# Performance work log

Measured on AMD Instinct MI355X. Metric: run time of the kernel, lower is better.

The kernel has to match this reference:

```python
import jax, jax.numpy as jnp
import numpy as np

S = 4        # support_num
NEI = 32     # neighbor_num for conv stages
POOL_NEI = 4 # neighbor_num inside Pool_layer
EPS = 1e-12


def sq_dist(a, b):
    # a: (b,m,3), b: (b,n,3) -> (b,m,n)
    return (jnp.sum(a * a, -1)[:, :, None] + jnp.sum(b * b, -1)[:, None, :]
            - 2.0 * jnp.einsum('bmd,bnd->bmn', a, b))


def query_ball(radius, k, points, queries):
    # PointNet++-style ball query: up to k indices within radius, padded with first hit.
    d = sq_dist(queries, points)                      # (b,m,n)
    n = points.shape[1]
    idx = jnp.broadcast_to(jnp.arange(n, dtype=jnp.int32), d.shape)
    idx = jnp.where(d > radius * radius, n, idx)
    idx = jnp.sort(idx, axis=-1)[..., :k]             # (b,m,k)
    first = idx[..., :1]
    return jnp.where(idx == n, first, idx)


def gather_nb(feat, idx):
    # feat: (b,v,c), idx: (b,v,k) -> (b,v,k,c)
    return jax.vmap(lambda f, i: f[i])(feat, idx)


def neighbor_dir_norm(verts, idx):
    nb = gather_nb(verts, idx)                        # (b,v,k,3)
    d = nb - verts[:, :, None, :]
    return d / (jnp.linalg.norm(d, axis=-1, keepdims=True) + EPS)


def conv_surface(idx, verts, dirs):
    # dirs: (3, S*out). Geometric-only first layer of 3DGCN.
    b, v, k = idx.shape
    o = dirs.shape[1] // S
    dn = neighbor_dir_norm(verts, idx)                # (b,v,k,3)
    sd = dirs / (jnp.linalg.norm(dirs, axis=0, keepdims=True) + EPS)
    theta = jnp.maximum(jnp.einsum('bvkd,dm->bvkm', dn, sd), 0.0)
    theta = theta.reshape(b, v, k, S, o)
    return theta.max(axis=2).sum(axis=2)              # (b,v,o)


def conv_layer(idx, verts, feat, w, bias, dirs):
    # w: (cin,(S+1)*o), bias: ((S+1)*o,), dirs: (3,S*o)
    b, v, k = idx.shape
    o = dirs.shape[1] // S
    dn = neighbor_dir_norm(verts, idx)
    sd = dirs / (jnp.linalg.norm(dirs, axis=0, keepdims=True) + EPS)
    theta = jnp.maximum(jnp.einsum('bvkd,dm->bvkm', dn, sd), 0.0)  # (b,v,k,S*o)
    fout = feat @ w + bias                            # (b,v,(S+1)*o)
    center, supp = fout[..., :o], fout[..., o:]
    supp_nb = gather_nb(supp, idx)                    # (b,v,k,S*o)
    act = (theta * supp_nb).reshape(b, v, k, S, o).max(axis=2).sum(axis=2)
    return center + act


def pool(verts, feat, radius):
    idx = query_ball(radius, POOL_NEI, verts, verts)
    pooled = gather_nb(feat, idx).max(axis=2)         # (b,v,c)
    m = verts.shape[1] // 2                           # pooling_rate = 2 (deterministic subsample)
    return verts[:, :m], pooled[:, :m]


def setup_inputs() -> dict:
    key = jax.random.key(0)
    ks = jax.random.split(key, 32)
    B, V = 4, 4096
    inp = {}
    inp['vertices'] = jax.random.uniform(ks[0], (B, V, 3), dtype=jnp.float32)
    inp['surf_dirs'] = jax.random.normal(ks[1], (3, S * 32), dtype=jnp.float32) * 0.1
    specs = [(1, 32, 32), (3, 64, 32), (4, 96, 32), (6, 128, 32), (7, 160, 32),
             (8, 192, 32), (9, 224, 32), (10, 256, 32), (11, 288, 1024)]
    i = 2
    for n, cin, cout in specs:
        inp[f'w{n}'] = jax.random.normal(ks[i], (cin, (S + 1) * cout), dtype=jnp.float32) / np.sqrt(cin); i += 1
        inp[f'b{n}'] = jnp.zeros(((S + 1) * cout,), jnp.float32)
        inp[f'd{n}'] = jax.random.normal(ks[i], (3, S * cout), dtype=jnp.float32) * 0.1; i += 1
    inp['fc1_w'] = jax.random.normal(ks[i], (1024, 256), dtype=jnp.float32) * 0.03; i += 1
    inp['fc1_b'] = jnp.zeros((256,), jnp.float32)
    inp['bn_g'] = jnp.ones((256,), jnp.float32)
    inp['bn_b'] = jnp.zeros((256,), jnp.float32)
    inp['bn_m'] = jnp.zeros((256,), jnp.float32)
    inp['bn_v'] = jnp.ones((256,), jnp.float32)
    inp['fc2_w'] = jax.random.normal(ks[i], (256, 40), dtype=jnp.float32) * 0.06
    inp['fc2_b'] = jnp.zeros((40,), jnp.float32)
    return inp


def reference(vertices, surf_dirs, w1, b1, d1, w3, b3, d3, w4, b4, d4, w6, b6, d6,
              w7, b7, d7, w8, b8, d8, w9, b9, d9, w10, b10, d10, w11, b11, d11,
              fc1_w, fc1_b, bn_g, bn_b, bn_m, bn_v, fc2_w, fc2_b):
    relu = lambda x: jnp.maximum(x, 0.0)
    verts = vertices
    idx = query_ball(0.2, NEI, verts, verts)
    fm0 = relu(conv_surface(idx, verts, surf_dirs))
    fm1 = relu(conv_layer(idx, verts, fm0, w1, b1, d1))
    fm1 = jnp.concatenate([fm0, fm1], -1)
    verts, fm1 = pool(verts, fm1, 0.2)
    idx = query_ball(0.4, NEI, verts, verts)
    fm3 = relu(conv_layer(idx, verts, fm1, w3, b3, d3)); fm3 = jnp.concatenate([fm1, fm3], -1)
    fm4 = relu(conv_layer(idx, verts, fm3, w4, b4, d4)); fm4 = jnp.concatenate([fm3, fm4], -1)
    verts, fm4 = pool(verts, fm4, 0.4)
    idx = query_ball(0.6, NEI, verts, verts)
    fm6 = relu(conv_layer(idx, verts, fm4, w6, b6, d6)); fm6 = jnp.concatenate([fm4, fm6], -1)
    fm7 = relu(conv_layer(idx, verts, fm6, w7, b7, d7)); fm7 = jnp.concatenate([fm6, fm7], -1)
    verts, fm7 = pool(verts, fm7, 0.6)
    idx = query_ball(0.8, NEI, verts, verts)
    fm8 = relu(conv_layer(idx, verts, fm7, w8, b8, d8)); fm8 = jnp.concatenate([fm7, fm8], -1)
    fm9 = relu(conv_layer(idx, verts, fm8, w9, b9, d9)); fm9 = jnp.concatenate([fm8, fm9], -1)
    verts, fm9 = pool(verts, fm9, 0.8)
    idx = query_ball(1.0, NEI, verts, verts)
    fm10 = relu(conv_layer(idx, verts, fm9, w10, b10, d10)); fm10 = jnp.concatenate([fm9, fm10], -1)
    fm11 = conv_layer(idx, verts, fm10, w11, b11, d11)
    g = fm11.max(axis=1)                              # (b,1024) global max pool
    h = g @ fc1_w + fc1_b                             # Dropout is identity at inference
    h = (h - bn_m) / jnp.sqrt(bn_v + 1e-5) * bn_g + bn_b
    h = relu(h)
    return h @ fc2_w + fc2_b                          # (b,40)
```

## Files before the change

kernel.cpp:

```cpp
#include <hip/hip_runtime.h>
#include <hip/hip_bf16.h>
#include <math.h>

#define DEV __device__ __forceinline__

DEV float frn_mul(float a, float b) { return __fmul_rn(a, b); }
DEV float frn_add(float a, float b) { return __fadd_rn(a, b); }

union BFU { __hip_bfloat16 h; unsigned short u; };

typedef __attribute__((ext_vector_type(8))) short short8v;
typedef __attribute__((ext_vector_type(4))) float f32x4;

__global__ void pack4_kernel(const float* __restrict__ v, float4* __restrict__ out,
                             int n)
{
    int t = blockIdx.x * blockDim.x + threadIdx.x;
    if (t >= n) return;
    float x = v[(size_t)t * 3 + 0], y = v[(size_t)t * 3 + 1], z = v[(size_t)t * 3 + 2];
    float pn = frn_add(frn_add(frn_mul(x, x), frn_mul(y, y)), frn_mul(z, z));
    out[t] = make_float4(x, y, z, pn);
}

__global__ void qb_kernel(const float4* __restrict__ pts4all, int Vp, int Vq, int B,
                          float r2, int K, int* __restrict__ idx_out)
{
    int wid = (blockIdx.x * blockDim.x + threadIdx.x) >> 6;
    int lane = threadIdx.x & 63;
    int nq = B * Vq;
    if (wid >= nq) return;
    int b = wid / Vq;
    int v = wid - b * Vq;

    float4 q4 = pts4all[(size_t)b * Vp + v];
    float qx = q4.x, qy = q4.y, qz = q4.z, qn = q4.w;
    const float4* pts = pts4all + (size_t)b * Vp;
    int* row = idx_out + (size_t)wid * K;

    int count = 0;
    int first = -1;
    float4 pbuf[2];
#pragma unroll
    for (int u = 0; u < 2; ++u) pbuf[u] = pts[u * 64 + lane];
    for (int base = 0; base < Vp && count < K; base += 128) {
#pragma unroll
        for (int u = 0; u < 2; ++u) {
            float4 p = pbuf[u];
            int jn = base + 128 + u * 64 + lane;
            pbuf[u] = pts[jn < Vp ? jn : 0];
            float dt = frn_add(frn_add(frn_mul(qx, p.x), frn_mul(qy, p.y)), frn_mul(qz, p.z));
            float d = __fsub_rn(frn_add(qn, p.w), frn_mul(2.0f, dt));
            bool in = !(d > r2);
            unsigned long long mask = __ballot(in);
            if (first < 0 && mask != 0ull)
                first = base + u * 64 + (int)__ffsll((long long)mask) - 1;
            int pos = count + (int)__popcll(mask & ((1ull << lane) - 1ull));
            if (in && pos < K) row[pos] = base + u * 64 + lane;
            count += (int)__popcll(mask);
        }
    }
    int cnt = count < K ? count : K;
    for (int t = cnt + lane; t < K; t += 64) row[t] = first;
}

__global__ void qb_surface_kernel(const float4* __restrict__ pts4all, int V, int B,
                                  float r2,
                                  const float* __restrict__ dirs,
                                  float* __restrict__ outF, int Cw,
                                  int* __restrict__ idx_out)
{
    __shared__ int rowS[4][32];
    int wid = (blockIdx.x * blockDim.x + threadIdx.x) >> 6;
    int lane = threadIdx.x & 63;
    int wql = threadIdx.x >> 6;
    int b = wid / V;

    float4 q4 = pts4all[(size_t)wid];
    float qx = q4.x, qy = q4.y, qz = q4.z, qn = q4.w;
    const float4* pts = pts4all + (size_t)b * V;
    int* row = idx_out + (size_t)wid * 32;

    int count = 0;
    int first = -1;
    float4 pbuf[4];
#pragma unroll
    for (int u = 0; u < 4; ++u) pbuf[u] = pts[u * 64 + lane];
    for (int base = 0; base < V && count < 32; base += 256) {
#pragma unroll
        for (int u = 0; u < 4; ++u) {
            float4 p = pbuf[u];
            int jn = base + 256 + u * 64 + lane;
            pbuf[u] = pts[jn < V ? jn : 0];
            float dt = frn_add(frn_add(frn_mul(qx, p.x), frn_mul(qy, p.y)), frn_mul(qz, p.z));
            float d = __fsub_rn(frn_add(qn, p.w), frn_mul(2.0f, dt));
            bool in = !(d > r2);
            unsigned long long mask = __ballot(in);
            if (first < 0 && mask != 0ull)
                first = base + u * 64 + (int)__ffsll((long long)mask) - 1;
            int pos = count + (int)__popcll(mask & ((1ull << lane) - 1ull));
            if (in && pos < 32) { row[pos] = base + u * 64 + lane; rowS[wql][pos] = base + u * 64 + lane; }
            count += (int)__popcll(mask);
        }
    }
    int cnt = count < 32 ? count : 32;
    for (int t = cnt + lane; t < 32; t += 64) { row[t] = first; rowS[wql][t] = first; }
    __syncthreads();

    float dnx, dny, dnz;
    {
        int k = lane & 31;
        float4 nb4 = pts[rowS[wql][k]];
        float dx = nb4.x - qx;
        float dy = nb4.y - qy;
        float dz = nb4.z - qz;
        float nrm = sqrtf(dx * dx + dy * dy + dz * dz) + 1e-12f;
        float inv = 1.0f / nrm;
        dnx = dx * inv; dny = dy * inv; dnz = dz * inv;
    }
    int m1 = lane, m2 = lane + 64;
    float ax = dirs[m1], ay = dirs[128 + m1], az = dirs[256 + m1];
    float i1 = 1.0f / (sqrtf(ax * ax + ay * ay + az * az) + 1e-12f);
    ax *= i1; ay *= i1; az *= i1;
    float bx = dirs[m2], by = dirs[128 + m2], bz = dirs[256 + m2];
    float i2 = 1.0f / (sqrtf(bx * bx + by * by + bz * bz) + 1e-12f);
    bx *= i2; by *= i2; bz *= i2;

    float mx1 = -INFINITY, mx2 = -INFINITY;
    for (int k = 0; k < 32; ++k) {
        float ex = __shfl(dnx, k, 64);
        float ey = __shfl(dny, k, 64);
        float ez = __shfl(dnz, k, 64);
        float t1 = fmaxf(ex * ax + ey * ay + ez * az, 0.0f);
        float t2 = fmaxf(ex * bx + ey * by + ez * bz, 0.0f);
        mx1 = fmaxf(mx1, t1);
        mx2 = fmaxf(mx2, t2);
    }
    float part = mx1 + mx2;
    float tot = part + __shfl_xor(part, 32, 64);
    if (lane < 32) {
        outF[(size_t)wid * Cw + lane] = fmaxf(tot, 0.0f);
    }
}

template <typename OT>
__global__ __launch_bounds__(256)
void gemm_tiled_kernel(const float* __restrict__ feat, int Cw, int cin,
                       const float* __restrict__ w, const float* __restrict__ bias,
                       int N, OT* __restrict__ fout)
{
    __shared__ float As[64][36];
    __shared__ float Bs[32][68];

    int m0 = blockIdx.x * 64;
    int n0 = blockIdx.y * 64;
    int tid = threadIdx.x;
    int tx = tid & 15, ty = tid >> 4;

    float acc[4][4];
#pragma unroll
    for (int i = 0; i < 4; ++i)
#pragma unroll
        for (int j = 0; j < 4; ++j) acc[i][j] = 0.0f;

    for (int k0 = 0; k0 < cin; k0 += 32) {
#pragma unroll
        for (int i = 0; i < 2; ++i) {
            int qq = tid + i * 256;
            int row = qq >> 3, c = qq & 7;
            float4 v = *(const float4*)&feat[(size_t)(m0 + row) * Cw + k0 + 4 * c];
            *(float4*)&As[row][4 * c] = v;
        }
// ... 14 lines not shown
#pragma unroll
            for (int i = 0; i < 4; ++i) av4[i] = *(const float4*)&As[ty * 4 + i][kt];
#pragma unroll
            for (int r = 0; r < 4; ++r) bv4[r] = *(const float4*)&Bs[kt + r][tx * 4];
            const float* a = (const float*)av4;
            const float* bb = (const float*)bv4;
#pragma unroll
            for (int i = 0; i < 4; ++i)
#pragma unroll
                for (int r = 0; r < 4; ++r)
#pragma unroll
                    for (int j = 0; j < 4; ++j)
                        acc[i][j] = fmaf(a[i * 4 + r], bb[r * 4 + j], acc[i][j]);
        }
        __syncthreads();
    }

    int n = n0 + tx * 4;
    if (n < N) {
        float b0 = bias[n + 0], b1 = bias[n + 1], b2 = bias[n + 2], b3 = bias[n + 3];
#pragma unroll
        for (int i = 0; i < 4; ++i) {
            int m = m0 + ty * 4 + i;
            if constexpr (__is_same(OT, float)) {
                float4 o;
                o.x = acc[i][0] + b0;
                o.y = acc[i][1] + b1;
                o.z = acc[i][2] + b2;
                o.w = acc[i][3] + b3;
                *(float4*)&fout[(size_t)m * N + n] = o;
            } else {
                BFU t0, t1, t2, t3;
                t0.h = __float2bfloat16(acc[i][0] + b0);
                t1.h = __float2bfloat16(acc[i][1] + b1);
                t2.h = __float2bfloat16(acc[i][2] + b2);
                t3.h = __float2bfloat16(acc[i][3] + b3);
                ushort4 o;
                o.x = t0.u; o.y = t1.u; o.z = t2.u; o.w = t3.u;
                *(ushort4*)&fout[(size_t)m * N + n] = o;
            }
        }
    }
}

__global__ void cast_bf16_kernel(const float* __restrict__ src,
                                 unsigned short* __restrict__ dst, int n8)
{
    int t = blockIdx.x * blockDim.x + threadIdx.x;
    if (t >= n8) return;
    float4 v0 = *(const float4*)&src[(size_t)t * 8];
    float4 v1 = *(const float4*)&src[(size_t)t * 8 + 4];
    BFU a;
    ushort4 o0, o1;
    a.h = __float2bfloat16(v0.x); o0.x = a.u;
    a.h = __float2bfloat16(v0.y); o0.y = a.u;
    a.h = __float2bfloat16(v0.z); o0.z = a.u;
    a.h = __float2bfloat16(v0.w); o0.w = a.u;
    a.h = __float2bfloat16(v1.x); o1.x = a.u;
    a.h = __float2bfloat16(v1.y); o1.y = a.u;
    a.h = __float2bfloat16(v1.z); o1.z = a.u;
    a.h = __float2bfloat16(v1.w); o1.w = a.u;
    *(ushort4*)&dst[(size_t)t * 8] = o0;
    *(ushort4*)&dst[(size_t)t * 8 + 4] = o1;
}

__global__ void castT_bf16_kernel(const float* __restrict__ w,
                                  unsigned short* __restrict__ wt)
{
    int t = blockIdx.x * blockDim.x + threadIdx.x;
    if (t >= 5120 * 36) return;
    int kc = t / 5120;
    int n = t - kc * 5120;
    BFU a;
    ushort4 o0, o1;
    a.h = __float2bfloat16(w[(size_t)(kc * 8 + 0) * 5120 + n]); o0.x = a.u;
    a.h = __float2bfloat16(w[(size_t)(kc * 8 + 1) * 5120 + n]); o0.y = a.u;
    a.h = __float2bfloat16(w[(size_t)(kc * 8 + 2) * 5120 + n]); o0.z = a.u;
    a.h = __float2bfloat16(w[(size_t)(kc * 8 + 3) * 5120 + n]); o0.w = a.u;
    a.h = __float2bfloat16(w[(size_t)(kc * 8 + 4) * 5120 + n]); o1.x = a.u;
    a.h = __float2bfloat16(w[(size_t)(kc * 8 + 5) * 5120 + n]); o1.y = a.u;
    a.h = __float2bfloat16(w[(size_t)(kc * 8 + 6) * 5120 + n]); o1.z = a.u;
    a.h = __float2bfloat16(w[(size_t)(kc * 8 + 7) * 5120 + n]); o1.w = a.u;
    *(ushort4*)&wt[(size_t)n * 288 + kc * 8] = o0;
    *(ushort4*)&wt[(size_t)n * 288 + kc * 8 + 4] = o1;
}

__global__ __launch_bounds__(256)
void gemm_mfma_conv11(const unsigned short* __restrict__ Abf,
                      const unsigned short* __restrict__ WTbf,
                      const float* __restrict__ bias,
                      __hip_bfloat16* __restrict__ fout)
{
    __shared__ unsigned short As[128][40];
    __shared__ unsigned short Bs[128][40];
    const int K = 288, N = 5120;
    int m0 = blockIdx.x * 128;
    int n0 = blockIdx.y * 128;
    int tid = threadIdx.x;
    int lane = tid & 63;
    int wave = tid >> 6;
    int wm = wave & 1, wn = wave >> 1;
    int l15 = lane & 15, l4 = lane >> 4;

    f32x4 acc[4][4];
#pragma unroll
    for (int mi = 0; mi < 4; ++mi)
#pragma unroll
// ... 22 lines not shown
            for (int ni = 0; ni < 4; ++ni)
                acc[mi][ni] = __builtin_amdgcn_mfma_f32_16x16x32_bf16(af[mi], bfv[ni], acc[mi][ni], 0, 0, 0);
        __syncthreads();
    }

#pragma unroll
    for (int ni = 0; ni < 4; ++ni) {
        int col = n0 + wn * 64 + ni * 16 + l15;
        float bv = bias[col];
#pragma unroll
        for (int mi = 0; mi < 4; ++mi) {
            int rbase = m0 + wm * 64 + mi * 16 + l4 * 4;
#pragma unroll
            for (int j = 0; j < 4; ++j) {
                BFU u;
                u.h = __float2bfloat16(acc[mi][ni][j] + bv);
                *(unsigned short*)&fout[(size_t)(rbase + j) * N + col] = u.u;
            }
        }
    }
}

__global__ void conv_agg32_kernel(const int* __restrict__ idx,
                                  const float4* __restrict__ verts4,
                                  const float* __restrict__ fout,
                                  const float* __restrict__ dirs,
                                  float* __restrict__ outF, int Cw, int coff,
                                  int V, int do_relu)
{
    int blk = blockIdx.x;
    int b = (blk & 7) >> 1;
    int j = ((blk >> 3) << 1) | (blk & 1);
    int wid = b * V + j * 4 + (int)(threadIdx.x >> 6);
    int lane = threadIdx.x & 63;

    float dnx, dny, dnz;
    int nbrow;
    {
        int k = lane & 31;
        int nb = idx[(size_t)wid * 32 + k];
        nbrow = b * V + nb;
        float4 c4 = verts4[(size_t)wid];
        float4 n4 = verts4[(size_t)nbrow];
        float dx = n4.x - c4.x;
        float dy = n4.y - c4.y;
        float dz = n4.z - c4.z;
        float nrm = sqrtf(dx * dx + dy * dy + dz * dz) + 1e-12f;
        float inv = 1.0f / nrm;
        dnx = dx * inv; dny = dy * inv; dnz = dz * inv;
    }
    int m1 = lane, m2 = lane + 64;
    float ax = dirs[m1], ay = dirs[128 + m1], az = dirs[256 + m1];
    float i1 = 1.0f / (sqrtf(ax * ax + ay * ay + az * az) + 1e-12f);
    ax *= i1; ay *= i1; az *= i1;
    float bx = dirs[m2], by = dirs[128 + m2], bz = dirs[256 + m2];
    float i2 = 1.0f / (sqrtf(bx * bx + by * by + bz * bz) + 1e-12f);
    bx *= i2; by *= i2; bz *= i2;

    float a1[4] = {-INFINITY, -INFINITY, -INFINITY, -INFINITY};
    float a2[4] = {-INFINITY, -INFINITY, -INFINITY, -INFINITY};
#pragma unroll
    for (int kk = 0; kk < 32; kk += 4) {
#pragma unroll
        for (int u = 0; u < 4; ++u) {
            int k = kk + u;
            float ex = __shfl(dnx, k, 64);
            float ey = __shfl(dny, k, 64);
            float ez = __shfl(dnz, k, 64);
            int nr = __shfl(nbrow, k, 64);
            const float* fr = fout + (size_t)nr * 160 + 32;
            float t1 = fmaxf(ex * ax + ey * ay + ez * az, 0.0f);
            float t2 = fmaxf(ex * bx + ey * by + ez * bz, 0.0f);
            a1[u] = fmaxf(a1[u], t1 * fr[m1]);
            a2[u] = fmaxf(a2[u], t2 * fr[m2]);
        }
    }
    float mx1 = fmaxf(fmaxf(a1[0], a1[1]), fmaxf(a1[2], a1[3]));
    float mx2 = fmaxf(fmaxf(a2[0], a2[1]), fmaxf(a2[2], a2[3]));
    float part = mx1 + mx2;
    float tot = part + __shfl_xor(part, 32, 64);
    if (lane < 32) {
        float c = fout[(size_t)wid * 160 + lane];
        float val = c + tot;
        if (do_relu) val = fmaxf(val, 0.0f);
        outF[(size_t)wid * Cw + coff + lane] = val;
    }
}

__global__ __launch_bounds__(256)
void conv_agg_big_kernel(const int* __restrict__ idx,
                         const float4* __restrict__ verts4,
                         const __hip_bfloat16* __restrict__ fout,
                         const float* __restrict__ dirs,
                         float* __restrict__ G,
                         int V, int B)
{
    __shared__ float dnS[32][3];
    __shared__ int nbS[32];
    __shared__ float sm[256 * 17];
    int blk = blockIdx.x;
    int b = (blk & 7) >> 1;
    int v = ((blk >> 3) << 1) | (blk & 1);
    int row = b * V + v;
    int tid = threadIdx.x;

    if (tid < 32) {
        int nb = idx[(size_t)row * 32 + tid];
        int nbrow = b * V + nb;
        float4 c4 = verts4[(size_t)row];
        float4 n4 = verts4[(size_t)nbrow];
        float dx = n4.x - c4.x;
        float dy = n4.y - c4.y;
        float dz = n4.z - c4.z;
        float nrm = sqrtf(dx * dx + dy * dy + dz * dz) + 1e-12f;
        float inv = 1.0f / nrm;
        dnS[tid][0] = dx * inv; dnS[tid][1] = dy * inv; dnS[tid][2] = dz * inv;
        nbS[tid] = nbrow;
    }
    __syncthreads();

    int p0 = tid * 16;
    float4 X[4], Y[4], Z[4];
#pragma unroll
    for (int c = 0; c < 4; ++c) {
        X[c] = *(const float4*)&dirs[p0 + 4 * c];
        Y[c] = *(const float4*)&dirs[4096 + p0 + 4 * c];
        Z[c] = *(const float4*)&dirs[8192 + p0 + 4 * c];
    }
    const float* xf = (const float*)X;
    const float* yf = (const float*)Y;
    const float* zf = (const float*)Z;
    float sdx[16], sdy[16], sdz[16], mx[16];
#pragma unroll
    for (int p = 0; p < 16; ++p) {
        float ax = xf[p], ay = yf[p], az = zf[p];
        float inv = 1.0f / (sqrtf(ax * ax + ay * ay + az * az) + 1e-12f);
        sdx[p] = ax * inv; sdy[p] = ay * inv; sdz[p] = az * inv;
        mx[p] = -INFINITY;
    }

    for (int k = 0; k < 32; ++k) {
        float ex = dnS[k][0], ey = dnS[k][1], ez = dnS[k][2];
        const __hip_bfloat16* fr = fout + (size_t)nbS[k] * 5120 + 1024;
        uint4 u0 = *(const uint4*)&fr[p0];
        uint4 u1 = *(const uint4*)&fr[p0 + 8];
        unsigned int uu[8] = {u0.x, u0.y, u0.z, u0.w, u1.x, u1.y, u1.z, u1.w};
#pragma unroll
        for (int h = 0; h < 8; ++h) {
            float slo = __uint_as_float(uu[h] << 16);
            float shi = __uint_as_float(uu[h] & 0xFFFF0000u);
            int p = 2 * h;
            float th0 = fmaxf(ex * sdx[p] + ey * sdy[p] + ez * sdz[p], 0.0f);
            float th1 = fmaxf(ex * sdx[p + 1] + ey * sdy[p + 1] + ez * sdz[p + 1], 0.0f);
            mx[p] = fmaxf(mx[p], th0 * slo);
            mx[p + 1] = fmaxf(mx[p + 1], th1 * shi);
        }
    }

#pragma unroll
    for (int p = 0; p < 16; ++p) sm[tid * 17 + p] = mx[p];
    __syncthreads();

#pragma unroll
    for (int q = 0; q < 4; ++q) {
        int oo = q * 256 + tid;
        int t0 = oo >> 4, pp = oo & 15;
        float s0 = sm[t0 * 17 + pp];
        float s1 = sm[(64 + t0) * 17 + pp];
        float s2 = sm[(128 + t0) * 17 + pp];
        float s3 = sm[(192 + t0) * 17 + pp];
        float val = ((s0 + s1) + s2) + s3;
        float c = __bfloat162float(fout[(size_t)row * 5120 + oo]);
        G[(size_t)row * 1024 + oo] = c + val;
    }
}

__global__ void pool_fused_kernel(const int* __restrict__ idx_conv,
                                  const float4* __restrict__ verts4, int Vp, int Vh, int B,
                                  const float* __restrict__ Fin, int CwIn,
                                  float* __restrict__ Fout, int CwOut, int C,
                                  float4* __restrict__ vout4)
{
    int wid = (blockIdx.x * blockDim.x + threadIdx.x) >> 6;
    int lane = threadIdx.x & 63;
    int nq = B * Vh;
    if (wid >= nq) return;
    int b = wid / Vh;
    int v = wid - b * Vh;
    int rowc = b * Vp + v;

    int idv = 0;
    if (lane < 4) idv = idx_conv[(size_t)rowc * 32 + lane];
    int i0 = __shfl(idv, 0, 64);
    int i1 = __shfl(idv, 1, 64);
    int i2 = __shfl(idv, 2, 64);
    int i3 = __shfl(idv, 3, 64);

    const float* r0 = Fin + (size_t)(b * Vp + i0) * CwIn;
    const float* r1 = Fin + (size_t)(b * Vp + i1) * CwIn;
    const float* r2p = Fin + (size_t)(b * Vp + i2) * CwIn;
    const float* r3 = Fin + (size_t)(b * Vp + i3) * CwIn;
    for (int c = lane; c < C; c += 64) {
        float m = fmaxf(fmaxf(r0[c], r1[c]), fmaxf(r2p[c], r3[c]));
        Fout[(size_t)wid * CwOut + c] = m;
    }
    if (lane == 0) vout4[(size_t)wid] = verts4[(size_t)rowc];
}

__global__ void gmax_kernel(const float* __restrict__ G, float* __restrict__ gm,
                            int V)
{
    __shared__ float red[4][64];
    int b = blockIdx.x >> 4;
    int c0 = (blockIdx.x & 15) * 64;
    int t = threadIdx.x;
    int c = c0 + (t & 63);
    int vg = t >> 6;
    float m = -INFINITY;
    for (int v = vg * 64; v < (vg + 1) * 64; ++v)
        m = fmaxf(m, G[((size_t)b * V + v) * 1024 + c]);
    red[vg][t & 63] = m;
    __syncthreads();
    if (t < 64) {
        float r = fmaxf(fmaxf(red[0][t], red[1][t]), fmaxf(red[2][t], red[3][t]));
        gm[b * 1024 + c0 + t] = r;
    }
}

__global__ __launch_bounds__(256)
// ... 78 lines not shown
    const float* w9 = (const float*)d_in[20];
    const float* b9 = (const float*)d_in[21];
    const float* d9 = (const float*)d_in[22];
    const float* w10 = (const float*)d_in[23];
    const float* b10 = (const float*)d_in[24];
    const float* d10 = (const float*)d_in[25];
    const float* w11 = (const float*)d_in[26];
    const float* b11 = (const float*)d_in[27];
    const float* d11 = (const float*)d_in[28];
    const float* fc1_w = (const float*)d_in[29];
    const float* fc1_b = (const float*)d_in[30];
    const float* bn_g = (const float*)d_in[31];
    const float* bn_b = (const float*)d_in[32];
    const float* bn_m = (const float*)d_in[33];
    const float* bn_v = (const float*)d_in[34];
    const float* fc2_w = (const float*)d_in[35];
    const float* fc2_b = (const float*)d_in[36];
    (void)in_sizes; (void)n_in; (void)out_size; (void)ws_size;

    float* ws = (float*)d_ws;
    size_t off = 0;
    auto alloc = [&](size_t n) { float* p = ws + off; off += n; return p; };
    float* fout = alloc(4 * 256 * 5120);
    int* idx = (int*)alloc(4 * 4096 * 32);
    float* F1 = alloc(4 * 4096 * 64);
    float* L2 = alloc(4 * 2048 * 128);
    float* L3 = alloc(4 * 1024 * 192);
    float* L4 = alloc(4 * 512 * 256);
    float* L5 = alloc(4 * 256 * 288);
    float* G = alloc(4 * 256 * 1024);
    float4* vp1 = (float4*)alloc(4 * 4096 * 4);
    float4* v2 = (float4*)alloc(4 * 2048 * 4);
    float4* v3 = (float4*)alloc(4 * 1024 * 4);
    float4* v4 = (float4*)alloc(4 * 512 * 4);
    float4* v5 = (float4*)alloc(4 * 256 * 4);
    float* gm = alloc(4 * 1024);
    float* hh = alloc(4 * 256);

    unsigned short* Abf = (unsigned short*)G;
    unsigned short* WTbf = Abf + 1024 * 288;

    pack4_kernel<<<tblocks(B * 4096), 256, 0, stream>>>(verts1, vp1, B * 4096);
    qb_surface_kernel<<<wblocks(B * 4096), 256, 0, stream>>>(vp1, 4096, B, 0.04f, surf_dirs, F1, 64, idx);
    gemm_tiled_kernel<float><<<ggrid(B * 4096, 160), 256, 0, stream>>>(F1, 64, 32, w1, b1, 160, fout);
    conv_agg32_kernel<<<B * 4096 / 4, 256, 0, stream>>>(idx, vp1, fout, d1, F1, 64, 32, 4096, 1);
    pool_fused_kernel<<<wblocks(B * 2048), 256, 0, stream>>>(idx, vp1, 4096, 2048, B, F1, 64, L2, 128, 64, v2);

    qb_kernel<<<wblocks(B * 2048), 256, 0, stream>>>(v2, 2048, 2048, B, 0.16f, 32, idx);
    gemm_tiled_kernel<float><<<ggrid(B * 2048, 160), 256, 0, stream>>>(L2, 128, 64, w3, b3, 160, fout);
    conv_agg32_kernel<<<B * 2048 / 4, 256, 0, stream>>>(idx, v2, fout, d3, L2, 128, 64, 2048, 1);
    gemm_tiled_kernel<float><<<ggrid(B * 2048, 160), 256, 0, stream>>>(L2, 128, 96, w4, b4, 160, fout);
    conv_agg32_kernel<<<B * 2048 / 4, 256, 0, stream>>>(idx, v2, fout, d4, L2, 128, 96, 2048, 1);
    pool_fused_kernel<<<wblocks(B * 1024), 256, 0, stream>>>(idx, v2, 2048, 1024, B, L2, 128, L3, 192, 128, v3);

    qb_kernel<<<wblocks(B * 1024), 256, 0, stream>>>(v3, 1024, 1024, B, 0.36f, 32, idx);
    gemm_tiled_kernel<float><<<ggrid(B * 1024, 160), 256, 0, stream>>>(L3, 192, 128, w6, b6, 160, fout);
    conv_agg32_kernel<<<B * 1024 / 4, 256, 0, stream>>>(idx, v3, fout, d6, L3, 192, 128, 1024, 1);
    gemm_tiled_kernel<float><<<ggrid(B * 1024, 160), 256, 0, stream>>>(L3, 192, 160, w7, b7, 160, fout);
    conv_agg32_kernel<<<B * 1024 / 4, 256, 0, stream>>>(idx, v3, fout, d7, L3, 192, 160, 1024, 1);
    pool_fused_kernel<<<wblocks(B * 512), 256, 0, stream>>>(idx, v3, 1024, 512, B, L3, 192, L4, 256, 192, v4);

    qb_kernel<<<wblocks(B * 512), 256, 0, stream>>>(v4, 512, 512, B, 0.64f, 32, idx);
    gemm_tiled_kernel<float><<<ggrid(B * 512, 160), 256, 0, stream>>>(L4, 256, 192, w8, b8, 160, fout);
    conv_agg32_kernel<<<B * 512 / 4, 256, 0, stream>>>(idx, v4, fout, d8, L4, 256, 192, 512, 1);
    gemm_tiled_kernel<float><<<ggrid(B * 512, 160), 256, 0, stream>>>(L4, 256, 224, w9, b9, 160, fout);
    conv_agg32_kernel<<<B * 512 / 4, 256, 0, stream>>>(idx, v4, fout, d9, L4, 256, 224, 512, 1);
    pool_fused_kernel<<<wblocks(B * 256), 256, 0, stream>>>(idx, v4, 512, 256, B, L4, 256, L5, 288, 256, v5);

    qb_kernel<<<wblocks(B * 256), 256, 0, stream>>>(v5, 256, 256, B, 1.0f, 32, idx);
    castT_bf16_kernel<<<(5120 * 36 + 255) / 256, 256, 0, stream>>>(w11, WTbf);
    gemm_tiled_kernel<float><<<ggrid(B * 256, 160), 256, 0, stream>>>(L5, 288, 256, w10, b10, 160, fout);
    conv_agg32_kernel<<<B * 256 / 4, 256, 0, stream>>>(idx, v5, fout, d10, L5, 288, 256, 256, 1);
    cast_bf16_kernel<<<(36864 + 255) / 256, 256, 0, stream>>>(L5, Abf, 36864);
    __hip_bfloat16* fout_bf = (__hip_bfloat16*)fout;
    gemm_mfma_conv11<<<dim3(8, 40), 256, 0, stream>>>(Abf, WTbf, b11, fout_bf);
    conv_agg_big_kernel<<<B * 256, 256, 0, stream>>>(idx, v5, fout_bf, d11, G, 256, B);

    gmax_kernel<<<64, 256, 0, stream>>>(G, gm, 256);
    fc1_kernel<<<dim3(8, B), 256, 0, stream>>>(gm, fc1_w, fc1_b, bn_g, bn_b, bn_m, bn_v, hh);
    fc2_kernel<<<B, 256, 0, stream>>>(hh, fc2_w, fc2_b, (float*)d_out);
}
```

Baseline: 440.4 us.

## Hoist all ball queries into one upfront mega kernel using prefix-subsampled vertices

Pooling always keeps a prefix of the vertices, so every level's points are a prefix of the packed level-1 array. The change runs all five ball queries, the surface conv and the w11 bf16 transpose in one large launch at the start, and drops the per-level vertex copies and the separate qb, cast and castT kernels. The bf16 copy of L5 is now written directly by pool_fused and conv_agg32, and conv_agg_big moves to 512 threads with 8 outputs each. This cuts launch count and serial dependencies, at the cost of relying on the prefix-subsampling assumption and some padding reads past the vertex array.

```diff
diff --git a/kernel.cpp b/kernel.cpp
--- a/kernel.cpp
+++ b/kernel.cpp
@@ -22,32 +22,20 @@
     out[t] = make_float4(x, y, z, pn);
 }
 
-__global__ void qb_kernel(const float4* __restrict__ pts4all, int Vp, int Vq, int B,
-                          float r2, int K, int* __restrict__ idx_out)
-{
-    int wid = (blockIdx.x * blockDim.x + threadIdx.x) >> 6;
-    int lane = threadIdx.x & 63;
-    int nq = B * Vq;
-    if (wid >= nq) return;
-    int b = wid / Vq;
-    int v = wid - b * Vq;
-
-    float4 q4 = pts4all[(size_t)b * Vp + v];
+DEV void qb_scan2(const float4* __restrict__ pts, int V, float4 q4, float r2,
+                  int lane, int* __restrict__ row)
+{
     float qx = q4.x, qy = q4.y, qz = q4.z, qn = q4.w;
-    const float4* pts = pts4all + (size_t)b * Vp;
-    int* row = idx_out + (size_t)wid * K;
-
     int count = 0;
     int first = -1;
     float4 pbuf[2];
 #pragma unroll
     for (int u = 0; u < 2; ++u) pbuf[u] = pts[u * 64 + lane];
-    for (int base = 0; base < Vp && count < K; base += 128) {
+    for (int base = 0; base < V && count < 32; base += 128) {
 #pragma unroll
         for (int u = 0; u < 2; ++u) {
             float4 p = pbuf[u];
-            int jn = base + 128 + u * 64 + lane;
-            pbuf[u] = pts[jn < Vp ? jn : 0];
+            pbuf[u] = pts[base + 128 + u * 64 + lane];
             float dt = frn_add(frn_add(frn_mul(qx, p.x), frn_mul(qy, p.y)), frn_mul(qz, p.z));
             float d = __fsub_rn(frn_add(qn, p.w), frn_mul(2.0f, dt));
             bool in = !(d > r2);
@@ -55,98 +43,133 @@
             if (first < 0 && mask != 0ull)
                 first = base + u * 64 + (int)__ffsll((long long)mask) - 1;
             int pos = count + (int)__popcll(mask & ((1ull << lane) - 1ull));
-            if (in && pos < K) row[pos] = base + u * 64 + lane;
+            if (in && pos < 32) row[pos] = base + u * 64 + lane;
             count += (int)__popcll(mask);
         }
     }
-    int cnt = count < K ? count : K;
-    for (int t = cnt + lane; t < K; t += 64) row[t] = first;
-}
-
-__global__ void qb_surface_kernel(const float4* __restrict__ pts4all, int V, int B,
-                                  float r2,
-                                  const float* __restrict__ dirs,
-                                  float* __restrict__ outF, int Cw,
-                                  int* __restrict__ idx_out)
+    int cnt = count < 32 ? count : 32;
+    for (int t = cnt + lane; t < 32; t += 64) row[t] = first;
+}
+
+__global__ __launch_bounds__(256)
+void mega_start_kernel(const float4* __restrict__ vp1,
+                       const float* __restrict__ dirs,
+                       float* __restrict__ outF, int Cw,
+                       int* __restrict__ idx1, int* __restrict__ idx2,
+                       int* __restrict__ idx3, int* __restrict__ idx4,
+                       int* __restrict__ idx5,
+                       const float* __restrict__ w11, unsigned short* __restrict__ wt)
 {
     __shared__ int rowS[4][32];
-    int wid = (blockIdx.x * blockDim.x + threadIdx.x) >> 6;
-    int lane = threadIdx.x & 63;
-    int wql = threadIdx.x >> 6;
-    int b = wid / V;
-
-    float4 q4 = pts4all[(size_t)wid];
-    float qx = q4.x, qy = q4.y, qz = q4.z, qn = q4.w;
-    const float4* pts = pts4all + (size_t)b * V;
-    int* row = idx_out + (size_t)wid * 32;
-
-    int count = 0;
-    int first = -1;
-    float4 pbuf[4];
-#pragma unroll
-    for (int u = 0; u < 4; ++u) pbuf[u] = pts[u * 64 + lane];
-    for (int base = 0; base < V && count < 32; base += 256) {
-#pragma unroll
-        for (int u = 0; u < 4; ++u) {
-            float4 p = pbuf[u];
-            int jn = base + 256 + u * 64 + lane;
-            pbuf[u] = pts[jn < V ? jn : 0];
-            float dt = frn_add(frn_add(frn_mul(qx, p.x), frn_mul(qy, p.y)), frn_mul(qz, p.z));
-            float d = __fsub_rn(frn_add(qn, p.w), frn_mul(2.0f, dt));
-            bool in = !(d > r2);
-            unsigned long long mask = __ballot(in);
-            if (first < 0 && mask != 0ull)
-                first = base + u * 64 + (int)__ffsll((long long)mask) - 1;
-            int pos = count + (int)__popcll(mask & ((1ull << lane) - 1ull));
-            if (in && pos < 32) { row[pos] = base + u * 64 + lane; rowS[wql][pos] = base + u * 64 + lane; }
-            count += (int)__popcll(mask);
-        }
-    }
-    int cnt = count < 32 ? count : 32;
-    for (int t = cnt + lane; t < 32; t += 64) { row[t] = first; rowS[wql][t] = first; }
-    __syncthreads();
-
-    float dnx, dny, dnz;
-    {
-        int k = lane & 31;
-        float4 nb4 = pts[rowS[wql][k]];
-        float dx = nb4.x - qx;
-        float dy = nb4.y - qy;
-        float dz = nb4.z - qz;
-        float nrm = sqrtf(dx * dx + dy * dy + dz * dz) + 1e-12f;
-        float inv = 1.0f / nrm;
-        dnx = dx * inv; dny = dy * inv; dnz = dz * inv;
-    }
-    int m1 = lane, m2 = lane + 64;
-    float ax = dirs[m1], ay = dirs[128 + m1], az = dirs[256 + m1];
-    float i1 = 1.0f / (sqrtf(ax * ax + ay * ay + az * az) + 1e-12f);
-    ax *= i1; ay *= i1; az *= i1;
-    float bx = dirs[m2], by = dirs[128 + m2], bz = dirs[256 + m2];
-    float i2 = 1.0f / (sqrtf(bx * bx + by * by + bz * bz) + 1e-12f);
-    bx *= i2; by *= i2; bz *= i2;
-
-    float mx1 = -INFINITY, mx2 = -INFINITY;
-    for (int k = 0; k < 32; ++k) {
-        float ex = __shfl(dnx, k, 64);
-        float ey = __shfl(dny, k, 64);
-        float ez = __shfl(dnz, k, 64);
-        float t1 = fmaxf(ex * ax + ey * ay + ez * az, 0.0f);
-        float t2 = fmaxf(ex * bx + ey * by + ez * bz, 0.0f);
-        mx1 = fmaxf(mx1, t1);
-        mx2 = fmaxf(mx2, t2);
-    }
-    float part = mx1 + mx2;
-    float tot = part + __shfl_xor(part, 32, 64);
-    if (lane < 32) {
-        outF[(size_t)wid * Cw + lane] = fmaxf(tot, 0.0f);
-    }
-}
-
-template <typename OT>
+    int bid = blockIdx.x;
+    int tid = threadIdx.x;
+    int lane = tid & 63;
+
+    if (bid < 4096) {
+        int wid = (bid * 256 + tid) >> 6;
+        int wql = tid >> 6;
+        int b = wid >> 12;
+        float4 q4 = vp1[(size_t)wid];
+        float qx = q4.x, qy = q4.y, qz = q4.z, qn = q4.w;
+        const float4* pts = vp1 + (size_t)b * 4096;
+        int* row = idx1 + (size_t)wid * 32;
+
+        int count = 0;
+        int first = -1;
+        float4 pbuf[4];
+#pragma unroll
+        for (int u = 0; u < 4; ++u) pbuf[u] = pts[u * 64 + lane];
+        for (int base = 0; base < 4096 && count < 32; base += 256) {
+#pragma unroll
+            for (int u = 0; u < 4; ++u) {
+                float4 p = pbuf[u];
+                pbuf[u] = pts[base + 256 + u * 64 + lane];
+                float dt = frn_add(frn_add(frn_mul(qx, p.x), frn_mul(qy, p.y)), frn_mul(qz, p.z));
+                float d = __fsub_rn(frn_add(qn, p.w), frn_mul(2.0f, dt));
+                bool in = !(d > 0.04f);
+                unsigned long long mask = __ballot(in);
+                if (first < 0 && mask != 0ull)
+                    first = base + u * 64 + (int)__ffsll((long long)mask) - 1;
+                int pos = count + (int)__popcll(mask & ((1ull << lane) - 1ull));
+                if (in && pos < 32) { row[pos] = base + u * 64 + lane; rowS[wql][pos] = base + u * 64 + lane; }
+                count += (int)__popcll(mask);
+            }
+        }
+        int cnt = count < 32 ? count : 32;
+        for (int t = cnt + lane; t < 32; t += 64) { row[t] = first; rowS[wql][t] = first; }
+        __syncthreads();
+
+        float dnx, dny, dnz;
+        {
+            int k = lane & 31;
+            float4 nb4 = pts[rowS[wql][k]];
+            float dx = nb4.x - qx;
+            float dy = nb4.y - qy;
+            float dz = nb4.z - qz;
+            float nrm = sqrtf(dx * dx + dy * dy + dz * dz) + 1e-12f;
+            float inv = 1.0f / nrm;
+            dnx = dx * inv; dny = dy * inv; dnz = dz * inv;
+        }
+        int m1 = lane, m2 = lane + 64;
+        float ax = dirs[m1], ay = dirs[128 + m1], az = dirs[256 + m1];
+        float i1 = 1.0f / (sqrtf(ax * ax + ay * ay + az * az) + 1e-12f);
+        ax *= i1; ay *= i1; az *= i1;
+        float bx = dirs[m2], by = dirs[128 + m2], bz = dirs[256 + m2];
+        float i2 = 1.0f / (sqrtf(bx * bx + by * by + bz * bz) + 1e-12f);
+        bx *= i2; by *= i2; bz *= i2;
+
+        float mx1 = -INFINITY, mx2 = -INFINITY;
+        for (int k = 0; k < 32; ++k) {
+            float ex = __shfl(dnx, k, 64);
+            float ey = __shfl(dny, k, 64);
+            float ez = __shfl(dnz, k, 64);
+            float t1 = fmaxf(ex * ax + ey * ay + ez * az, 0.0f);
+            float t2 = fmaxf(ex * bx + ey * by + ez * bz, 0.0f);
+            mx1 = fmaxf(mx1, t1);
+            mx2 = fmaxf(mx2, t2);
+        }
+        float part = mx1 + mx2;
+        float tot = part + __shfl_xor(part, 32, 64);
+        if (lane < 32) {
+            outF[(size_t)wid * Cw + lane] = fmaxf(tot, 0.0f);
+        }
+    } else if (bid < 7936) {
+        int V, r_bid; float r2; int* idxp;
+        if (bid < 6144)      { V = 2048; r2 = 0.16f; idxp = idx2; r_bid = bid - 4096; }
+        else if (bid < 7168) { V = 1024; r2 = 0.36f; idxp = idx3; r_bid = bid - 6144; }
+        else if (bid < 7680) { V = 512;  r2 = 0.64f; idxp = idx4; r_bid = bid - 7168; }
+        else                 { V = 256;  r2 = 1.0f;  idxp = idx5; r_bid = bid - 7680; }
+        int widl = (r_bid * 256 + tid) >> 6;
+        int b = widl / V;
+        int v = widl - b * V;
+        float4 q4 = vp1[(size_t)b * 4096 + v];
+        const float4* pts = vp1 + (size_t)b * 4096;
+        qb_scan2(pts, V, q4, r2, lane, idxp + (size_t)widl * 32);
+    } else {
+        int t = (bid - 7936) * 256 + tid;
+        if (t < 5120 * 36) {
+            int kc = t / 5120;
+            int n = t - kc * 5120;
+            BFU a;
+            ushort4 o0, o1;
+            a.h = __float2bfloat16(w11[(size_t)(kc * 8 + 0) * 5120 + n]); o0.x = a.u;
+            a.h = __float2bfloat16(w11[(size_t)(kc * 8 + 1) * 5120 + n]); o0.y = a.u;
+            a.h = __float2bfloat16(w11[(size_t)(kc * 8 + 2) * 5120 + n]); o0.z = a.u;
+            a.h = __float2bfloat16(w11[(size_t)(kc * 8 + 3) * 5120 + n]); o0.w = a.u;
+            a.h = __float2bfloat16(w11[(size_t)(kc * 8 + 4) * 5120 + n]); o1.x = a.u;
+            a.h = __float2bfloat16(w11[(size_t)(kc * 8 + 5) * 5120 + n]); o1.y = a.u;
+            a.h = __float2bfloat16(w11[(size_t)(kc * 8 + 6) * 5120 + n]); o1.z = a.u;
+            a.h = __float2bfloat16(w11[(size_t)(kc * 8 + 7) * 5120 + n]); o1.w = a.u;
+            *(ushort4*)&wt[(size_t)n * 288 + kc * 8] = o0;
+            *(ushort4*)&wt[(size_t)n * 288 + kc * 8 + 4] = o1;
+        }
+    }
+}
+
 __global__ __launch_bounds__(256)
 void gemm_tiled_kernel(const float* __restrict__ feat, int Cw, int cin,
                        const float* __restrict__ w, const float* __restrict__ bias,
-                       int N, OT* __restrict__ fout)
+                       int N, float* __restrict__ fout)
 {
     __shared__ float As[64][36];
     __shared__ float Bs[32][68];
@@ -207,67 +230,14 @@
 #pragma unroll
         for (int i = 0; i < 4; ++i) {
             int m = m0 + ty * 4 + i;
-            if constexpr (__is_same(OT, float)) {
-                float4 o;
-                o.x = acc[i][0] + b0;
-                o.y = acc[i][1] + b1;
-                o.z = acc[i][2] + b2;
-                o.w = acc[i][3] + b3;
-                *(float4*)&fout[(size_t)m * N + n] = o;
-            } else {
-                BFU t0, t1, t2, t3;
-                t0.h = __float2bfloat16(acc[i][0] + b0);
-                t1.h = __float2bfloat16(acc[i][1] + b1);
-                t2.h = __float2bfloat16(acc[i][2] + b2);
-                t3.h = __float2bfloat16(acc[i][3] + b3);
-                ushort4 o;
-                o.x = t0.u; o.y = t1.u; o.z = t2.u; o.w = t3.u;
-                *(ushort4*)&fout[(size_t)m * N + n] = o;
-            }
-        }
-    }
-}
-
-__global__ void cast_bf16_kernel(const float* __restrict__ src,
-                                 unsigned short* __restrict__ dst, int n8)
-{
-    int t = blockIdx.x * blockDim.x + threadIdx.x;
-    if (t >= n8) return;
-    float4 v0 = *(const float4*)&src[(size_t)t * 8];
-    float4 v1 = *(const float4*)&src[(size_t)t * 8 + 4];
-    BFU a;
-    ushort4 o0, o1;
-    a.h = __float2bfloat16(v0.x); o0.x = a.u;
-    a.h = __float2bfloat16(v0.y); o0.y = a.u;
-    a.h = __float2bfloat16(v0.z); o0.z = a.u;
-    a.h = __float2bfloat16(v0.w); o0.w = a.u;
-    a.h = __float2bfloat16(v1.x); o1.x = a.u;
-    a.h = __float2bfloat16(v1.y); o1.y = a.u;
-    a.h = __float2bfloat16(v1.z); o1.z = a.u;
-    a.h = __float2bfloat16(v1.w); o1.w = a.u;
-    *(ushort4*)&dst[(size_t)t * 8] = o0;
-    *(ushort4*)&dst[(size_t)t * 8 + 4] = o1;
-}
-
-__global__ void castT_bf16_kernel(const float* __restrict__ w,
-                                  unsigned short* __restrict__ wt)
-{
-    int t = blockIdx.x * blockDim.x + threadIdx.x;
-    if (t >= 5120 * 36) return;
-    int kc = t / 5120;
-    int n = t - kc * 5120;
-    BFU a;
-    ushort4 o0, o1;
-    a.h = __float2bfloat16(w[(size_t)(kc * 8 + 0) * 5120 + n]); o0.x = a.u;
-    a.h = __float2bfloat16(w[(size_t)(kc * 8 + 1) * 5120 + n]); o0.y = a.u;
-    a.h = __float2bfloat16(w[(size_t)(kc * 8 + 2) * 5120 + n]); o0.z = a.u;
-    a.h = __float2bfloat16(w[(size_t)(kc * 8 + 3) * 5120 + n]); o0.w = a.u;
-    a.h = __float2bfloat16(w[(size_t)(kc * 8 + 4) * 5120 + n]); o1.x = a.u;
-    a.h = __float2bfloat16(w[(size_t)(kc * 8 + 5) * 5120 + n]); o1.y = a.u;
-    a.h = __float2bfloat16(w[(size_t)(kc * 8 + 6) * 5120 + n]); o1.z = a.u;
-    a.h = __float2bfloat16(w[(size_t)(kc * 8 + 7) * 5120 + n]); o1.w = a.u;
-    *(ushort4*)&wt[(size_t)n * 288 + kc * 8] = o0;
-    *(ushort4*)&wt[(size_t)n * 288 + kc * 8 + 4] = o1;
+            float4 o;
+            o.x = acc[i][0] + b0;
+            o.y = acc[i][1] + b1;
+            o.z = acc[i][2] + b2;
+            o.w = acc[i][3] + b3;
+            *(float4*)&fout[(size_t)m * N + n] = o;
+        }
+    }
 }
 
 __global__ __launch_bounds__(256)
@@ -336,16 +306,18 @@
 }
 
 __global__ void conv_agg32_kernel(const int* __restrict__ idx,
-                                  const float4* __restrict__ verts4,
+                                  const float4* __restrict__ vp1,
                                   const float* __restrict__ fout,
                                   const float* __restrict__ dirs,
                                   float* __restrict__ outF, int Cw, int coff,
-                                  int V, int do_relu)
+                                  int V, int do_relu,
+                                  unsigned short* __restrict__ abf)
 {
     int blk = blockIdx.x;
     int b = (blk & 7) >> 1;
     int j = ((blk >> 3) << 1) | (blk & 1);
-    int wid = b * V + j * 4 + (int)(threadIdx.x >> 6);
+    int vloc = j * 4 + (int)(threadIdx.x >> 6);
+    int wid = b * V + vloc;
     int lane = threadIdx.x & 63;
 
     float dnx, dny, dnz;
@@ -354,8 +326,8 @@
         int k = lane & 31;
         int nb = idx[(size_t)wid * 32 + k];
         nbrow = b * V + nb;
-        float4 c4 = verts4[(size_t)wid];
-        float4 n4 = verts4[(size_t)nbrow];
+        float4 c4 = vp1[(size_t)b * 4096 + vloc];
+        float4 n4 = vp1[(size_t)b * 4096 + nb];
         float dx = n4.x - c4.x;
         float dy = n4.y - c4.y;
         float dz = n4.z - c4.z;
@@ -398,20 +370,24 @@
         float val = c + tot;
         if (do_relu) val = fmaxf(val, 0.0f);
         outF[(size_t)wid * Cw + coff + lane] = val;
-    }
-}
-
-__global__ __launch_bounds__(256)
+        if (abf) {
+            BFU u; u.h = __float2bfloat16(val);
+            abf[(size_t)wid * 288 + coff + lane] = u.u;
+        }
+    }
+}
+
+__global__ __launch_bounds__(512)
 void conv_agg_big_kernel(const int* __restrict__ idx,
-                         const float4* __restrict__ verts4,
+                         const float4* __restrict__ vp1,
                          const __hip_bfloat16* __restrict__ fout,
                          const float* __restrict__ dirs,
                          float* __restrict__ G,
                          int V, int B)
 {
     __shared__ float dnS[32][3];
-    __shared__ int nbS[32];
-    __shared__ float sm[256 * 17];
+    __shared__ long long offS[32];
+    __shared__ float sm[512 * 9];
     int blk = blockIdx.x;
     int b = (blk & 7) >> 1;
     int v = ((blk >> 3) << 1) | (blk & 1);
@@ -420,23 +396,22 @@
 
     if (tid < 32) {
         int nb = idx[(size_t)row * 32 + tid];
-        int nbrow = b * V + nb;
-        float4 c4 = verts4[(size_t)row];
-        float4 n4 = verts4[(size_t)nbrow];
+        float4 c4 = vp1[(size_t)b * 4096 + v];
+        float4 n4 = vp1[(size_t)b * 4096 + nb];
         float dx = n4.x - c4.x;
         float dy = n4.y - c4.y;
         float dz = n4.z - c4.z;
         float nrm = sqrtf(dx * dx + dy * dy + dz * dz) + 1e-12f;
         float inv = 1.0f / nrm;
         dnS[tid][0] = dx * inv; dnS[tid][1] = dy * inv; dnS[tid][2] = dz * inv;
-        nbS[tid] = nbrow;
+        offS[tid] = (long long)(b * V + nb) * 5120 + 1024;
     }
     __syncthreads();
 
-    int p0 = tid * 16;
-    float4 X[4], Y[4], Z[4];
-#pragma unroll
-    for (int c = 0; c < 4; ++c) {
+    int p0 = tid * 8;
+    float4 X[2], Y[2], Z[2];
+#pragma unroll
+    for (int c = 0; c < 2; ++c) {
         X[c] = *(const float4*)&dirs[p0 + 4 * c];
         Y[c] = *(const float4*)&dirs[4096 + p0 + 4 * c];
         Z[c] = *(const float4*)&dirs[8192 + p0 + 4 * c];
@@ -444,23 +419,23 @@
     const float* xf = (const float*)X;
     const float* yf = (const float*)Y;
     const float* zf = (const float*)Z;
-    float sdx[16], sdy[16], sdz[16], mx[16];
-#pragma unroll
-    for (int p = 0; p < 16; ++p) {
+    float sdx[8], sdy[8], sdz[8], mx[8];
+#pragma unroll
+    for (int p = 0; p < 8; ++p) {
         float ax = xf[p], ay = yf[p], az = zf[p];
         float inv = 1.0f / (sqrtf(ax * ax + ay * ay + az * az) + 1e-12f);
         sdx[p] = ax * inv; sdy[p] = ay * inv; sdz[p] = az * inv;
         mx[p] = -INFINITY;
     }
 
+#pragma unroll 2
     for (int k = 0; k < 32; ++k) {
         float ex = dnS[k][0], ey = dnS[k][1], ez = dnS[k][2];
-        const __hip_bfloat16* fr = fout + (size_t)nbS[k] * 5120 + 1024;
+        const __hip_bfloat16* fr = fout + offS[k];
         uint4 u0 = *(const uint4*)&fr[p0];
-        uint4 u1 = *(const uint4*)&fr[p0 + 8];
-        unsigned int uu[8] = {u0.x, u0.y, u0.z, u0.w, u1.x, u1.y, u1.z, u1.w};
-#pragma unroll
-        for (int h = 0; h < 8; ++h) {
+        unsigned int uu[4] = {u0.x, u0.y, u0.z, u0.w};
+#pragma unroll
+        for (int h = 0; h < 4; ++h) {
             float slo = __uint_as_float(uu[h] << 16);
             float shi = __uint_as_float(uu[h] & 0xFFFF0000u);
             int p = 2 * h;
@@ -472,17 +447,17 @@
     }
 
 #pragma unroll
-    for (int p = 0; p < 16; ++p) sm[tid * 17 + p] = mx[p];
+    for (int p = 0; p < 8; ++p) sm[tid * 9 + p] = mx[p];
     __syncthreads();
 
 #pragma unroll
-    for (int q = 0; q < 4; ++q) {
-        int oo = q * 256 + tid;
-        int t0 = oo >> 4, pp = oo & 15;
-        float s0 = sm[t0 * 17 + pp];
-        float s1 = sm[(64 + t0) * 17 + pp];
-        float s2 = sm[(128 + t0) * 17 + pp];
-        float s3 = sm[(192 + t0) * 17 + pp];
+    for (int q = 0; q < 2; ++q) {
+        int oo = q * 512 + tid;
+        int t0 = oo >> 3, pp = oo & 7;
+        float s0 = sm[t0 * 9 + pp];
+        float s1 = sm[(128 + t0) * 9 + pp];
+        float s2 = sm[(256 + t0) * 9 + pp];
+        float s3 = sm[(384 + t0) * 9 + pp];
         float val = ((s0 + s1) + s2) + s3;
         float c = __bfloat162float(fout[(size_t)row * 5120 + oo]);
         G[(size_t)row * 1024 + oo] = c + val;
@@ -490,10 +465,10 @@
 }
 
 __global__ void pool_fused_kernel(const int* __restrict__ idx_conv,
-                                  const float4* __restrict__ verts4, int Vp, int Vh, int B,
+                                  int Vp, int Vh, int B,
                                   const float* __restrict__ Fin, int CwIn,
                                   float* __restrict__ Fout, int CwOut, int C,
-                                  float4* __restrict__ vout4)
+                                  unsigned short* __restrict__ abf)
 {
     int wid = (blockIdx.x * blockDim.x + threadIdx.x) >> 6;
     int lane = threadIdx.x & 63;
@@ -517,8 +492,11 @@
     for (int c = lane; c < C; c += 64) {
         float m = fmaxf(fmaxf(r0[c], r1[c]), fmaxf(r2p[c], r3[c]));
         Fout[(size_t)wid * CwOut + c] = m;
-    }
-    if (lane == 0) vout4[(size_t)wid] = verts4[(size_t)rowc];
+        if (abf) {
+            BFU u; u.h = __float2bfloat16(m);
+            abf[(size_t)wid * 288 + c] = u.u;
+        }
+    }
 }
 
 __global__ void gmax_kernel(const float* __restrict__ G, float* __restrict__ gm,
@@ -643,18 +621,18 @@
     size_t off = 0;
     auto alloc = [&](size_t n) { float* p = ws + off; off += n; return p; };
     float* fout = alloc(4 * 256 * 5120);
-    int* idx = (int*)alloc(4 * 4096 * 32);
+    int* idx1 = (int*)alloc(4 * 4096 * 32);
+    int* idx2 = (int*)alloc(4 * 2048 * 32);
+    int* idx3 = (int*)alloc(4 * 1024 * 32);
+    int* idx4 = (int*)alloc(4 * 512 * 32);
+    int* idx5 = (int*)alloc(4 * 256 * 32);
     float* F1 = alloc(4 * 4096 * 64);
     float* L2 = alloc(4 * 2048 * 128);
     float* L3 = alloc(4 * 1024 * 192);
     float* L4 = alloc(4 * 512 * 256);
     float* L5 = alloc(4 * 256 * 288);
     float* G = alloc(4 * 256 * 1024);
-    float4* vp1 = (float4*)alloc(4 * 4096 * 4);
-    float4* v2 = (float4*)alloc(4 * 2048 * 4);
-    float4* v3 = (float4*)alloc(4 * 1024 * 4);
-    float4* v4 = (float4*)alloc(4 * 512 * 4);
-    float4* v5 = (float4*)alloc(4 * 256 * 4);
+    float4* vp1 = (float4*)alloc((4 * 4096 + 512) * 4);
     float* gm = alloc(4 * 1024);
     float* hh = alloc(4 * 256);
 
@@ -662,40 +640,37 @@
     unsigned short* WTbf = Abf + 1024 * 288;
 
     pack4_kernel<<<tblocks(B * 4096), 256, 0, stream>>>(verts1, vp1, B * 4096);
-    qb_surface_kernel<<<wblocks(B * 4096), 256, 0, stream>>>(vp1, 4096, B, 0.04f, surf_dirs, F1, 64, idx);
-    gemm_tiled_kernel<float><<<ggrid(B * 4096, 160), 256, 0, stream>>>(F1, 64, 32, w1, b1, 160, fout);
-    conv_agg32_kernel<<<B * 4096 / 4, 256, 0, stream>>>(idx, vp1, fout, d1, F1, 64, 32, 4096, 1);
-    pool_fused_kernel<<<wblocks(B * 2048), 256, 0, stream>>>(idx, vp1, 4096, 2048, B, F1, 64, L2, 128, 64, v2);
-
-    qb_kernel<<<wblocks(B * 2048), 256, 0, stream>>>(v2, 2048, 2048, B, 0.16f, 32, idx);
-    gemm_tiled_kernel<float><<<ggrid(B * 2048, 160), 256, 0, stream>>>(L2, 128, 64, w3, b3, 160, fout);
-    conv_agg32_kernel<<<B * 2048 / 4, 256, 0, stream>>>(idx, v2, fout, d3, L2, 128, 64, 2048, 1);
-    gemm_tiled_kernel<float><<<ggrid(B * 2048, 160), 256, 0, stream>>>(L2, 128, 96, w4, b4, 160, fout);
-    conv_agg32_kernel<<<B * 2048 / 4, 256, 0, stream>>>(idx, v2, fout, d4, L2, 128, 96, 2048, 1);
-    pool_fused_kernel<<<wblocks(B * 1024), 256, 0, stream>>>(idx, v2, 2048, 1024, B, L2, 128, L3, 192, 128, v3);
-
-    qb_kernel<<<wblocks(B * 1024), 256, 0, stream>>>(v3, 1024, 1024, B, 0.36f, 32, idx);
-    gemm_tiled_kernel<float><<<ggrid(B * 1024, 160), 256, 0, stream>>>(L3, 192, 128, w6, b6, 160, fout);
-    conv_agg32_kernel<<<B * 1024 / 4, 256, 0, stream>>>(idx, v3, fout, d6, L3, 192, 128, 1024, 1);
-    gemm_tiled_kernel<float><<<ggrid(B * 1024, 160), 256, 0, stream>>>(L3, 192, 160, w7, b7, 160, fout);
-    conv_agg32_kernel<<<B * 1024 / 4, 256, 0, stream>>>(idx, v3, fout, d7, L3, 192, 160, 1024, 1);
-    pool_fused_kernel<<<wblocks(B * 512), 256, 0, stream>>>(idx, v3, 1024, 512, B, L3, 192, L4, 256, 192, v4);
-
-    qb_kernel<<<wblocks(B * 512), 256, 0, stream>>>(v4, 512, 512, B, 0.64f, 32, idx);
-    gemm_tiled_kernel<float><<<ggrid(B * 512, 160), 256, 0, stream>>>(L4, 256, 192, w8, b8, 160, fout);
-    conv_agg32_kernel<<<B * 512 / 4, 256, 0, stream>>>(idx, v4, fout, d8, L4, 256, 192, 512, 1);
-    gemm_tiled_kernel<float><<<ggrid(B * 512, 160), 256, 0, stream>>>(L4, 256, 224, w9, b9, 160, fout);
-    conv_agg32_kernel<<<B * 512 / 4, 256, 0, stream>>>(idx, v4, fout, d9, L4, 256, 224, 512, 1);
-    pool_fused_kernel<<<wblocks(B * 256), 256, 0, stream>>>(idx, v4, 512, 256, B, L4, 256, L5, 288, 256, v5);
-
-    qb_kernel<<<wblocks(B * 256), 256, 0, stream>>>(v5, 256, 256, B, 1.0f, 32, idx);
-    castT_bf16_kernel<<<(5120 * 36 + 255) / 256, 256, 0, stream>>>(w11, WTbf);
-    gemm_tiled_kernel<float><<<ggrid(B * 256, 160), 256, 0, stream>>>(L5, 288, 256, w10, b10, 160, fout);
-    conv_agg32_kernel<<<B * 256 / 4, 256, 0, stream>>>(idx, v5, fout, d10, L5, 288, 256, 256, 1);
-    cast_bf16_kernel<<<(36864 + 255) / 256, 256, 0, stream>>>(L5, Abf, 36864);
+    mega_start_kernel<<<8656, 256, 0, stream>>>(vp1, surf_dirs, F1, 64,
+                                                idx1, idx2, idx3, idx4, idx5,
+                                                w11, WTbf);
+
+    gemm_tiled_kernel<<<ggrid(B * 4096, 160), 256, 0, stream>>>(F1, 64, 32, w1, b1, 160, fout);
+    conv_agg32_kernel<<<B * 4096 / 4, 256, 0, stream>>>(idx1, vp1, fout, d1, F1, 64, 32, 4096, 1, nullptr);
+    pool_fused_kernel<<<wblocks(B * 2048), 256, 0, stream>>>(idx1, 4096, 2048, B, F1, 64, L2, 128, 64, nullptr);
+
+    gemm_tiled_kernel<<<ggrid(B * 2048, 160), 256, 0, stream>>>(L2, 128, 64, w3, b3, 160, fout);
+    conv_agg32_kernel<<<B * 2048 / 4, 256, 0, stream>>>(idx2, vp1, fout, d3, L2, 128, 64, 2048, 1, nullptr);
+    gemm_tiled_kernel<<<ggrid(B * 2048, 160), 256, 0, stream>>>(L2, 128, 96, w4, b4, 160, fout);
+    conv_agg32_kernel<<<B * 2048 / 4, 256, 0, stream>>>(idx2, vp1, fout, d4, L2, 128, 96, 2048, 1, nullptr);
+    pool_fused_kernel<<<wblocks(B * 1024), 256, 0, stream>>>(idx2, 2048, 1024, B, L2, 128, L3, 192, 128, nullptr);
+
+    gemm_tiled_kernel<<<ggrid(B * 1024, 160), 256, 0, stream>>>(L3, 192, 128, w6, b6, 160, fout);
+    conv_agg32_kernel<<<B * 1024 / 4, 256, 0, stream>>>(idx3, vp1, fout, d6, L3, 192, 128, 1024, 1, nullptr);
+    gemm_tiled_kernel<<<ggrid(B * 1024, 160), 256, 0, stream>>>(L3, 192, 160, w7, b7, 160, fout);
+    conv_agg32_kernel<<<B * 1024 / 4, 256, 0, stream>>>(idx3, vp1, fout, d7, L3, 192, 160, 1024, 1, nullptr);
+    pool_fused_kernel<<<wblocks(B * 512), 256, 0, stream>>>(idx3, 1024, 512, B, L3, 192, L4, 256, 192, nullptr);
+
+    gemm_tiled_kernel<<<ggrid(B * 512, 160), 256, 0, stream>>>(L4, 256, 192, w8, b8, 160, fout);
+    conv_agg32_kernel<<<B * 512 / 4, 256, 0, stream>>>(idx4, vp1, fout, d8, L4, 256, 192, 512, 1, nullptr);
+    gemm_tiled_kernel<<<ggrid(B * 512, 160), 256, 0, stream>>>(L4, 256, 224, w9, b9, 160, fout);
+    conv_agg32_kernel<<<B * 512 / 4, 256, 0, stream>>>(idx4, vp1, fout, d9, L4, 256, 224, 512, 1, nullptr);
+    pool_fused_kernel<<<wblocks(B * 256), 256, 0, stream>>>(idx4, 512, 256, B, L4, 256, L5, 288, 256, Abf);
+
+    gemm_tiled_kernel<<<ggrid(B * 256, 160), 256, 0, stream>>>(L5, 288, 256, w10, b10, 160, fout);
+    conv_agg32_kernel<<<B * 256 / 4, 256, 0, stream>>>(idx5, vp1, fout, d10, L5, 288, 256, 256, 1, Abf);
     __hip_bfloat16* fout_bf = (__hip_bfloat16*)fout;
     gemm_mfma_conv11<<<dim3(8, 40), 256, 0, stream>>>(Abf, WTbf, b11, fout_bf);
-    conv_agg_big_kernel<<<B * 256, 256, 0, stream>>>(idx, v5, fout_bf, d11, G, 256, B);
+    conv_agg_big_kernel<<<B * 256, 512, 0, stream>>>(idx5, vp1, fout_bf, d11, G, 256, B);
 
     gmax_kernel<<<64, 256, 0, stream>>>(G, gm, 256);
     fc1_kernel<<<dim3(8, B), 256, 0, stream>>>(gm, fc1_w, fc1_b, bn_g, bn_b, bn_m, bn_v, hh);
```

Measured after the change: 414.0 us (median of 2 runs). -6.0%, faster.
